# Performance work log

Measured on AMD Instinct MI355X. Metric: run time of the kernel, lower is better.

The kernel has to match this reference:

```python
import jax, jax.numpy as jnp
import numpy as np

B, T, D, H, E, DLAT = 4, 2048, 512, 8, 32, 64
DH = D // H  # head_dim = 64


def rmsnorm(x, gamma, eps=1e-6):
    norm = jnp.sqrt(jnp.mean(jnp.square(x), axis=-1, keepdims=True) + eps)
    return gamma * (x / norm)


def apply_rope(x):
    # x: (B, T, H, Dh); rotate-half style RoPE over last dim
    _, t, _, d = x.shape
    inv_freq = 1.0 / (10000.0 ** (jnp.arange(0, d, 2, dtype=jnp.float32) / d))
    freqs = jnp.outer(jnp.arange(t, dtype=jnp.float32), inv_freq)  # (T, d/2)
    sin = jnp.sin(freqs)[None, :, None, :]
    cos = jnp.cos(freqs)[None, :, None, :]
    x1, x2 = jnp.split(x, 2, axis=-1)
    return jnp.concatenate([x1 * cos - x2 * sin, x1 * sin + x2 * cos], axis=-1)


def setup_inputs() -> dict:
    key = jax.random.key(0)
    ks = jax.random.split(key, 8)
    s = lambda fan_in: 1.0 / np.sqrt(fan_in)
    return {
        "x": jax.random.normal(ks[0], (B, T, D), jnp.float32),
        "gamma1": jnp.ones((D,), jnp.float32),
        "gamma2": jnp.ones((D,), jnp.float32),
        "wq": jax.random.normal(ks[1], (D, D), jnp.float32) * s(D),
        "bq": jnp.zeros((D,), jnp.float32),
        "wkd": jax.random.normal(ks[2], (D, DLAT), jnp.float32) * s(D),
        "bkd": jnp.zeros((DLAT,), jnp.float32),
        "wku": jax.random.normal(ks[3], (DLAT, 2 * D), jnp.float32) * s(DLAT),
        "bku": jnp.zeros((2 * D,), jnp.float32),
        "wo": jax.random.normal(ks[4], (D, D), jnp.float32) * s(D),
        "bo": jnp.zeros((D,), jnp.float32),
        "wg": jax.random.normal(ks[5], (D, E), jnp.float32) * s(D),
        "bg": jnp.zeros((E,), jnp.float32),
        "expert_w": jax.random.normal(ks[6], (E, D, D), jnp.float32) * s(D),
    }


def reference(x, gamma1, gamma2, wq, bq, wkd, bkd, wku, bku, wo, bo, wg, bg, expert_w):
    b, t, d = x.shape
    # --- MLA attention branch ---
    h = rmsnorm(x, gamma1)
    q = (h @ wq + bq).reshape(b, t, H, DH)
    kv = ((h @ wkd + bkd) @ wku + bku).reshape(b, t, H, 2 * DH)
    k, v = jnp.split(kv, 2, axis=-1)
    q = apply_rope(q)
    k = apply_rope(k)
    # NOTE (faithful to source): attention is across HEADS per timestep -> (B,T,H,H)
    att = jnp.einsum("bthd,btgd->bthg", q, k) / jnp.sqrt(jnp.float32(DH))
    att = jax.nn.softmax(att, axis=-1)
    out = jnp.einsum("bthg,btgd->bthd", att, v).reshape(b, t, d)
    x = x + (out @ wo + bo)
    # --- dense soft-MoE branch ---
    h2 = rmsnorm(x, gamma2)
    gate = jax.nn.softmax(h2 @ wg + bg, axis=-1)  # (B, T, E)
    moe = jnp.einsum("btd,edf,bte->btf", h2, expert_w, gate)
    return x + moe
```

## Files before the change

kernel.cpp:

```cpp
#include <hip/hip_runtime.h>
#include <hip/hip_bf16.h>

#define B_ 4
#define T_ 2048
#define D_ 512
#define H_ 8
#define E_ 32
#define DLAT_ 64
#define DH_ 64
#define M_ (B_*T_)

typedef unsigned short u16;
typedef unsigned int u32;
typedef __bf16 bf16x8 __attribute__((ext_vector_type(8)));
typedef float f32x4 __attribute__((ext_vector_type(4)));

__device__ __forceinline__ float bf2f(u16 u) {
    union { u32 i; float f; } c; c.i = ((u32)u) << 16; return c.f;
}
__device__ __forceinline__ u16 f2bf(float f) {
    union { float f; u32 i; } c; c.f = f;
    u32 x = c.i; x += 0x7fffu + ((x >> 16) & 1u);
    return (u16)(x >> 16);
}
__device__ __forceinline__ u32 pack2(float a, float b) {
    return (u32)f2bf(a) | ((u32)f2bf(b) << 16);
}

__global__ __launch_bounds__(256) void transpose_f2b(
    const float* __restrict__ src, u16* __restrict__ dst,
    int R, int C, int dstStride, long srcBatchStride, int dstBatchOff)
{
    __shared__ float tile[32][33];
    const int z = blockIdx.z;
    const float* s = src + (long)z * srcBatchStride;
    const int c0 = blockIdx.x * 32, r0 = blockIdx.y * 32;
    const int tx = threadIdx.x, ty = threadIdx.y;
#pragma unroll
    for (int i = 0; i < 32; i += 8) {
        int r = r0 + ty + i, c = c0 + tx;
        if (r < R && c < C) tile[ty + i][tx] = s[(long)r * C + c];
    }
    __syncthreads();
#pragma unroll
    for (int i = 0; i < 32; i += 8) {
        int c = c0 + ty + i, r = r0 + tx;
        if (r < R && c < C)
            dst[(long)c * dstStride + (long)z * dstBatchOff + r] = f2bf(tile[tx][ty + i]);
    }
}

__global__ __launch_bounds__(256) void rmsnorm_k(
    const float* __restrict__ x, const float* __restrict__ gamma,
    float* __restrict__ of, u16* __restrict__ ob)
{
    const size_t row = blockIdx.x;
    const int t = threadIdx.x;
    const float* xr = x + row * D_;
    float2 v = *(const float2*)(xr + 2 * t);
    float ss = v.x * v.x + v.y * v.y;
#pragma unroll
    for (int off = 1; off < 64; off <<= 1) ss += __shfl_xor(ss, off, 64);
    __shared__ float wsum[4];
    if ((t & 63) == 0) wsum[t >> 6] = ss;
    __syncthreads();
    float tot = wsum[0] + wsum[1] + wsum[2] + wsum[3];
    float inv = rsqrtf(tot * (1.0f / D_) + 1e-6f);
    float o0 = v.x * inv * gamma[2 * t];
    float o1 = v.y * inv * gamma[2 * t + 1];
    if (of) *(float2*)(of + row * D_ + 2 * t) = make_float2(o0, o1);
    if (ob) *(u32*)(ob + row * D_ + 2 * t) = pack2(o0, o1);
}

__global__ __launch_bounds__(512, 4) void gemm8w(
    const u16* __restrict__ A, const u16* __restrict__ Bt,
    const float* __restrict__ bias, const float* __restrict__ resid,
    float* __restrict__ outF, u16* __restrict__ outB, int Ndim, int strideA, int K)
{
    __shared__ __align__(16) u16 lA[128][72];
    __shared__ __align__(16) u16 lB[128][72];
    const int t = threadIdx.x;
    const int lane = t & 63, wid = t >> 6;
    const int wr = wid >> 2, wc = wid & 3;
    const int rowBase = blockIdx.x * 128;
    const int colBase = blockIdx.y * 128;
    const int srow = t >> 3;
    const int scol = (t & 7) * 8;
    const int l15 = lane & 15;
    const int kreg = (lane >> 4) * 8;

    f32x4 acc[4][2] = {};

    for (int kb = 0; kb < K; kb += 64) {
#pragma unroll
        for (int i = 0; i < 2; ++i) {
            int r = srow + 64 * i;
            *(int4*)(&lA[r][scol]) =
                *(const int4*)(A + (size_t)(rowBase + r) * strideA + kb + scol);
            *(int4*)(&lB[r][scol]) =
                *(const int4*)(Bt + (size_t)(colBase + r) * K + kb + scol);
        }
        __syncthreads();
#pragma unroll
        for (int kk = 0; kk < 64; kk += 32) {
            const int ko = kk + kreg;
            bf16x8 af[4], bfr[2];
#pragma unroll
            for (int mi = 0; mi < 4; ++mi)
                af[mi] = *(const bf16x8*)(&lA[wr * 64 + mi * 16 + l15][ko]);
#pragma unroll
            for (int ni = 0; ni < 2; ++ni)
                bfr[ni] = *(const bf16x8*)(&lB[wc * 32 + ni * 16 + l15][ko]);
#pragma unroll
            for (int mi = 0; mi < 4; ++mi)
#pragma unroll
                for (int ni = 0; ni < 2; ++ni)
                    acc[mi][ni] = __builtin_amdgcn_mfma_f32_16x16x32_bf16(
                        af[mi], bfr[ni], acc[mi][ni], 0, 0, 0);
        }
        __syncthreads();
    }
#pragma unroll
    for (int mi = 0; mi < 4; ++mi)
#pragma unroll
        for (int ni = 0; ni < 2; ++ni)
#pragma unroll
            for (int r = 0; r < 4; ++r) {
                int grow = rowBase + wr * 64 + mi * 16 + (lane >> 4) * 4 + r;
                int gcol = colBase + wc * 32 + ni * 16 + l15;
                float v = acc[mi][ni][r];
                if (bias)  v += bias[gcol];
                if (resid) v += resid[(size_t)grow * Ndim + gcol];
                if (outF)  outF[(size_t)grow * Ndim + gcol] = v;
                if (outB)  outB[(size_t)grow * Ndim + gcol] = f2bf(v);
            }
}

#define KPS_ 4096
__global__ __launch_bounds__(512, 4) void moe256(
    const u16* __restrict__ A, const u16* __restrict__ Bt,
    const float* __restrict__ gate, const float* __restrict__ resid,
    float* __restrict__ part)
{
    __shared__ __align__(16) u16 lA[256][72];
    __shared__ __align__(16) u16 lB[128][72];
    const int t = threadIdx.x;
    const int lane = t & 63, wid = t >> 6;
    const int wr = wid >> 1, wc = wid & 1;
    const int rowBase = blockIdx.x * 256;
    const int colBase = blockIdx.y * 128;
    const int z = blockIdx.z;
    const int eBase = z * (KPS_ / 512);
    float* outF = part + (size_t)z * M_ * D_;
    const float* rz = (z == 0) ? resid : nullptr;
    const int srow = t >> 3;
    const int scol = (t & 7) * 8;
    const int l15 = lane & 15;
    const int kreg = (lane >> 4) * 8;

    f32x4 acc[4][4] = {};

    for (int ei = 0; ei < 8; ++ei) {
        const int e = eBase + ei;
        float g[4];
#pragma unroll
        for (int i = 0; i < 4; ++i)
            g[i] = gate[(size_t)(rowBase + srow + 64 * i) * E_ + e];
#pragma unroll 1
        for (int k8 = 0; k8 < 8; ++k8) {
            const int akb = k8 * 64;
            const int kb = e * 512 + akb;
#pragma unroll
            for (int i = 0; i < 4; ++i) {
                int r = srow + 64 * i;
                bf16x8 raw = *(const bf16x8*)(A + (size_t)(rowBase + r) * 512 + akb + scol);
                bf16x8 o;
#pragma unroll
                for (int j = 0; j < 8; ++j)
                    o[j] = (__bf16)((float)raw[j] * g[i]);
                *(bf16x8*)(&lA[r][scol]) = o;
            }
#pragma unroll
            for (int i = 0; i < 2; ++i) {
                int r = srow + 64 * i;
                *(int4*)(&lB[r][scol]) =
                    *(const int4*)(Bt + (size_t)(colBase + r) * (E_ * 512) + kb + scol);
            }
            __syncthreads();
#pragma unroll
            for (int kk = 0; kk < 64; kk += 32) {
                const int ko = kk + kreg;
                bf16x8 af[4], bfr[4];
#pragma unroll
                for (int mi = 0; mi < 4; ++mi)
                    af[mi] = *(const bf16x8*)(&lA[wr * 64 + mi * 16 + l15][ko]);
#pragma unroll
                for (int ni = 0; ni < 4; ++ni)
                    bfr[ni] = *(const bf16x8*)(&lB[wc * 64 + ni * 16 + l15][ko]);
#pragma unroll
                for (int mi = 0; mi < 4; ++mi)
#pragma unroll
                    for (int ni = 0; ni < 4; ++ni)
                        acc[mi][ni] = __builtin_amdgcn_mfma_f32_16x16x32_bf16(
                            af[mi], bfr[ni], acc[mi][ni], 0, 0, 0);
            }
            __syncthreads();
        }
    }
#pragma unroll
    for (int mi = 0; mi < 4; ++mi)
#pragma unroll
        for (int ni = 0; ni < 4; ++ni)
#pragma unroll
            for (int r = 0; r < 4; ++r) {
                int grow = rowBase + wr * 64 + mi * 16 + (lane >> 4) * 4 + r;
                int gcol = colBase + wc * 64 + ni * 16 + l15;
                float v = acc[mi][ni][r];
                if (rz) v += rz[(size_t)grow * D_ + gcol];
                outF[(size_t)grow * D_ + gcol] = v;
            }
}

__global__ __launch_bounds__(256) void gemm_bt(
    const u16* __restrict__ A, const u16* __restrict__ Bt,
    const float* __restrict__ bias, float* __restrict__ outF,
    u16* __restrict__ outB, int Ndim, int K)
{
    __shared__ __align__(16) u16 lA[128][72];
    __shared__ __align__(16) u16 lB[64][72];
    const int t = threadIdx.x;
    const int lane = t & 63, wid = t >> 6;
    const int rowBase = blockIdx.x * 128;
    const int colBase = blockIdx.y * 64;
    const int srow = t >> 3;
    const int skb = (t & 7) * 8;
    const int l15 = lane & 15;
    const int kreg = (lane >> 4) * 8;

    f32x4 accT[2][4] = {};

    for (int kb = 0; kb < K; kb += 64) {
#pragma unroll
        for (int i = 0; i < 4; ++i) {
            int r = srow + 32 * i;
            size_t grow = (size_t)(rowBase + r);
            *(int4*)(&lA[r][skb]) = *(const int4*)(A + grow * (size_t)K + kb + skb);
        }
#pragma unroll
        for (int i = 0; i < 2; ++i) {
            int n = srow + 32 * i;
            int gn = colBase + n;
            int4 v = {0, 0, 0, 0};
            if (gn < Ndim) v = *(const int4*)(Bt + (size_t)gn * K + kb + skb);
            *(int4*)(&lB[n][skb]) = v;
        }
        __syncthreads();
#pragma unroll
        for (int kk = 0; kk < 64; kk += 32) {
            const int ko = kk + kreg;
            bf16x8 af[2], bfr[4];
            af[0] = *(const bf16x8*)(&lA[wid * 32 + l15][ko]);
            af[1] = *(const bf16x8*)(&lA[wid * 32 + 16 + l15][ko]);
#pragma unroll
            for (int ni = 0; ni < 4; ++ni)
                bfr[ni] = *(const bf16x8*)(&lB[ni * 16 + l15][ko]);
#pragma unroll
            for (int mi = 0; mi < 2; ++mi)
#pragma unroll
                for (int ni = 0; ni < 4; ++ni)
                    accT[mi][ni] = __builtin_amdgcn_mfma_f32_16x16x32_bf16(
                        af[mi], bfr[ni], accT[mi][ni], 0, 0, 0);
        }
        __syncthreads();
    }
#pragma unroll
    for (int mi = 0; mi < 2; ++mi)
#pragma unroll
        for (int ni = 0; ni < 4; ++ni)
#pragma unroll
            for (int r = 0; r < 4; ++r) {
                int grow = rowBase + wid * 32 + mi * 16 + (lane >> 4) * 4 + r;
                int gcol = colBase + ni * 16 + l15;
                if (gcol < Ndim) {
                    float v = accT[mi][ni][r];
                    if (bias)  v += bias[gcol];
                    if (outF)  outF[(size_t)grow * Ndim + gcol] = v;
                    if (outB)  outB[(size_t)grow * Ndim + gcol] = f2bf(v);
                }
            }
}

__global__ __launch_bounds__(256) void gatefused_k(
    const u16* __restrict__ A, const u16* __restrict__ Bt,
    const float* __restrict__ bg, float* __restrict__ gate)
{
    __shared__ __align__(16) u16 lA[128][72];
    __shared__ __align__(16) u16 lB[32][72];
    const int t = threadIdx.x;
    const int lane = t & 63, wid = t >> 6;
    const int rowBase = blockIdx.x * 128;
    const int srow = t >> 3;
    const int skb = (t & 7) * 8;
    const int l15 = lane & 15;
    const int kreg = (lane >> 4) * 8;

    f32x4 accT[2][2] = {};

    for (int kb = 0; kb < 512; kb += 64) {
#pragma unroll
        for (int i = 0; i < 4; ++i) {
            int r = srow + 32 * i;
            *(int4*)(&lA[r][skb]) =
                *(const int4*)(A + (size_t)(rowBase + r) * 512 + kb + skb);
        }
        *(int4*)(&lB[srow][skb]) = *(const int4*)(Bt + (size_t)srow * 512 + kb + skb);
        __syncthreads();
#pragma unroll
        for (int kk = 0; kk < 64; kk += 32) {
            const int ko = kk + kreg;
            bf16x8 af[2], bfr[2];
            af[0] = *(const bf16x8*)(&lA[wid * 32 + l15][ko]);
            af[1] = *(const bf16x8*)(&lA[wid * 32 + 16 + l15][ko]);
#pragma unroll
            for (int ni = 0; ni < 2; ++ni)
                bfr[ni] = *(const bf16x8*)(&lB[ni * 16 + l15][ko]);
#pragma unroll
            for (int mi = 0; mi < 2; ++mi)
#pragma unroll
                for (int ni = 0; ni < 2; ++ni)
                    accT[mi][ni] = __builtin_amdgcn_mfma_f32_16x16x32_bf16(
                        af[mi], bfr[ni], accT[mi][ni], 0, 0, 0);
        }
        __syncthreads();
    }
#pragma unroll
    for (int mi = 0; mi < 2; ++mi)
#pragma unroll
        for (int r = 0; r < 4; ++r) {
            float v0 = accT[mi][0][r] + bg[l15];
            float v1 = accT[mi][1][r] + bg[16 + l15];
            float m = fmaxf(v0, v1);
#pragma unroll
            for (int off = 1; off < 16; off <<= 1) m = fmaxf(m, __shfl_xor(m, off, 64));
            float p0 = __expf(v0 - m), p1 = __expf(v1 - m);
            float den = p0 + p1;
#pragma unroll
            for (int off = 1; off < 16; off <<= 1) den += __shfl_xor(den, off, 64);
            float rinv = 1.0f / den;
            int grow = rowBase + wid * 32 + mi * 16 + (lane >> 4) * 4 + r;
            gate[(size_t)grow * E_ + l15] = p0 * rinv;
            gate[(size_t)grow * E_ + 16 + l15] = p1 * rinv;
        }
}

__global__ __launch_bounds__(256) void reduce4_k(
    const float* __restrict__ p, float* __restrict__ o, int n4)
{
    int i = blockIdx.x * 256 + threadIdx.x;
    const int stride = gridDim.x * 256;
    for (; i < n4; i += stride) {
        float4 v0 = ((const float4*)p)[i];
        float4 v1 = ((const float4*)p)[i + n4];
        float4 v2 = ((const float4*)p)[i + 2 * n4];
        float4 v3 = ((const float4*)p)[i + 3 * n4];
        float4 r;
        r.x = v0.x + v1.x + v2.x + v3.x;
        r.y = v0.y + v1.y + v2.y + v3.y;
        r.z = v0.z + v1.z + v2.z + v3.z;
        r.w = v0.w + v1.w + v2.w + v3.w;
        ((float4*)o)[i] = r;
    }
}

__global__ __launch_bounds__(256) void rope_build(float2* __restrict__ tab)
{
    int i = blockIdx.x * 256 + threadIdx.x;
    int tpos = i >> 5, j = i & 31;
    float inv = exp2f(-(float)j * (13.287712379549449f / 32.0f));
    float ang = (float)tpos * inv;
    float sn, cs;
    sincosf(ang, &sn, &cs);
    tab[i] = make_float2(cs, sn);
}

__global__ __launch_bounds__(64) void attn_k(
    const u16* __restrict__ q, const u16* __restrict__ kv,
    const float2* __restrict__ rope, u16* __restrict__ out)
{
    const int tok = blockIdx.x;
    const int tpos = tok & (T_ - 1);
    const int l = threadIdx.x;
    __shared__ float sq[8][65], sk[8][65], sv[8][65];
    __shared__ float satt[8][9];
    const int h = l >> 3;
    const int j0 = (l & 7) * 4;
    const u16* qr = q + (size_t)tok * 512;
    const u16* kr = kv + (size_t)tok * 1024;
#pragma unroll
    for (int jj = 0; jj < 4; ++jj) {
        int j = j0 + jj;
        float2 cssn = rope[tpos * 32 + j];
        float cs = cssn.x, sn = cssn.y;
        float q1 = bf2f(qr[h * 64 + j]), q2 = bf2f(qr[h * 64 + 32 + j]);
        sq[h][j] = q1 * cs - q2 * sn;
        sq[h][j + 32] = q1 * sn + q2 * cs;
        float k1 = bf2f(kr[h * 128 + j]), k2 = bf2f(kr[h * 128 + 32 + j]);
        sk[h][j] = k1 * cs - k2 * sn;
        sk[h][j + 32] = k1 * sn + k2 * cs;
        sv[h][j] = bf2f(kr[h * 128 + 64 + j]);
        sv[h][j + 32] = bf2f(kr[h * 128 + 96 + j]);
    }
    __syncthreads();
    const int g = l & 7;
    float s = 0.f;
#pragma unroll 8
    for (int c = 0; c < 64; ++c) s += sq[h][c] * sk[g][c];
    s *= 0.125f;
    float m = s;
#pragma unroll
    for (int off = 4; off; off >>= 1) m = fmaxf(m, __shfl_xor(m, off, 8));
    float p = __expf(s - m);
    float den = p;
#pragma unroll
    for (int off = 4; off; off >>= 1) den += __shfl_xor(den, off, 8);
    satt[h][g] = p / den;
    __syncthreads();
    const int c8 = (l & 7) * 8;
    float o[8] = {};
#pragma unroll
    for (int gg = 0; gg < 8; ++gg) {
        float a = satt[h][gg];
#pragma unroll
        for (int i = 0; i < 8; ++i) o[i] += a * sv[gg][c8 + i];
    }
    int4 pk;
    pk.x = pack2(o[0], o[1]); pk.y = pack2(o[2], o[3]);
    pk.z = pack2(o[4], o[5]); pk.w = pack2(o[6], o[7]);
    *(int4*)(out + (size_t)tok * 512 + h * 64 + c8) = pk;
}

extern "C" void kernel_launch(void* const* d_in, const int* in_sizes, int n_in,
                              void* d_out, int out_size, void* d_ws, size_t ws_size,
                              hipStream_t stream)
{
    const float* x      = (const float*)d_in[0];
    const float* gamma1 = (const float*)d_in[1];
    const float* gamma2 = (const float*)d_in[2];
    const float* wq     = (const float*)d_in[3];
    const float* bq     = (const float*)d_in[4];
    const float* wkd    = (const float*)d_in[5];
    const float* bkd    = (const float*)d_in[6];
    const float* wku    = (const float*)d_in[7];
    const float* bku    = (const float*)d_in[8];
    const float* wo     = (const float*)d_in[9];
    const float* bo     = (const float*)d_in[10];
    const float* wg     = (const float*)d_in[11];
    const float* bg     = (const float*)d_in[12];
    const float* expw   = (const float*)d_in[13];

    char* w = (char*)d_ws;
    size_t off = 0;
    auto alloc = [&](size_t bytes) -> void* {
        void* p = w + off; off += (bytes + 255) & ~(size_t)255; return p;
    };
    u16*   h_b    = (u16*)alloc((size_t)M_ * D_ * 2);
    u16*   kd_b   = (u16*)alloc((size_t)M_ * DLAT_ * 2);
    u16*   at_b   = (u16*)alloc((size_t)M_ * D_ * 2);
    u16*   h2_b   = (u16*)alloc((size_t)M_ * D_ * 2);
    u16*   q_b    = (u16*)alloc((size_t)M_ * D_ * 2);
    u16*   kv_b   = (u16*)alloc((size_t)M_ * 2 * D_ * 2);
    float* parts  = (float*)alloc((size_t)4 * M_ * D_ * 4);
    float* x1_f   = (float*)alloc((size_t)M_ * D_ * 4);
    float* gate_f = (float*)alloc((size_t)M_ * E_ * 4);
    float2* rope_t = (float2*)alloc((size_t)T_ * 32 * 8);
    u16*   wqT    = (u16*)alloc((size_t)D_ * D_ * 2);
    u16*   wkdT   = (u16*)alloc((size_t)D_ * DLAT_ * 2);
    u16*   wkuT   = (u16*)alloc((size_t)DLAT_ * 2 * D_ * 2);
    u16*   woT    = (u16*)alloc((size_t)D_ * D_ * 2);
    u16*   wgT    = (u16*)alloc((size_t)D_ * E_ * 2);
    u16*   expT   = (u16*)alloc((size_t)E_ * D_ * D_ * 2);
    (void)ws_size; (void)in_sizes; (void)n_in; (void)out_size;

    dim3 tb(32, 8);
    transpose_f2b<<<dim3(16, 16, 1), tb, 0, stream>>>(wq,  wqT,  512, 512, 512, 0L, 0);
    transpose_f2b<<<dim3(2, 16, 1),  tb, 0, stream>>>(wkd, wkdT, 512, 64,  512, 0L, 0);
    transpose_f2b<<<dim3(32, 2, 1),  tb, 0, stream>>>(wku, wkuT, 64, 1024, 64,  0L, 0);
    transpose_f2b<<<dim3(16, 16, 1), tb, 0, stream>>>(wo,  woT,  512, 512, 512, 0L, 0);
    transpose_f2b<<<dim3(1, 16, 1),  tb, 0, stream>>>(wg,  wgT,  512, 32,  512, 0L, 0);
    transpose_f2b<<<dim3(16, 16, 32), tb, 0, stream>>>(expw, expT, 512, 512, 16384,
                                                       (long)512 * 512, 512);
    rope_build<<<(T_ * 32) / 256, 256, 0, stream>>>(rope_t);
    rmsnorm_k<<<M_, 256, 0, stream>>>(x, gamma1, nullptr, h_b);
    gemm8w<<<dim3(64, 4), 512, 0, stream>>>(h_b, wqT, bq, nullptr, nullptr, q_b,
                                            512, 512, 512);
    gemm_bt<<<dim3(64, 1), 256, 0, stream>>>(h_b, wkdT, bkd, nullptr, kd_b, 64, 512);
    gemm8w<<<dim3(64, 8), 512, 0, stream>>>(kd_b, wkuT, bku, nullptr, nullptr, kv_b,
                                            1024, 64, 64);
    attn_k<<<M_, 64, 0, stream>>>(q_b, kv_b, rope_t, at_b);
    gemm8w<<<dim3(64, 4), 512, 0, stream>>>(at_b, woT, bo, x, x1_f, nullptr,
                                            512, 512, 512);
    rmsnorm_k<<<M_, 256, 0, stream>>>(x1_f, gamma2, nullptr, h2_b);
    gatefused_k<<<dim3(64, 1), 256, 0, stream>>>(h2_b, wgT, bg, gate_f);
    moe256<<<dim3(32, 4, 4), 512, 0, stream>>>(h2_b, expT, gate_f, x1_f, parts);
    reduce4_k<<<2048, 256, 0, stream>>>(parts, (float*)d_out, M_ * D_ / 4);
}
```

Baseline: 342.3 us.

## Merge weight prep launches, store MoE partials in bf16, batch attention tokens

Folds the six weight transposes and the RoPE table build into one prep kernel dispatched by block index, which removes several launch overheads. Three of the four MoE split-K partial outputs are now written and read as bf16 instead of fp32, which cuts partial-sum traffic at some cost in precision. The attention kernel processes four tokens per 256-thread block instead of one token per 64-thread block, which improves occupancy and scheduling.

```diff
diff --git a/kernel.cpp b/kernel.cpp
--- a/kernel.cpp
+++ b/kernel.cpp
@@ -27,15 +27,45 @@
     return (u32)f2bf(a) | ((u32)f2bf(b) << 16);
 }
 
-__global__ __launch_bounds__(256) void transpose_f2b(
-    const float* __restrict__ src, u16* __restrict__ dst,
-    int R, int C, int dstStride, long srcBatchStride, int dstBatchOff)
-{
+__global__ __launch_bounds__(256) void prep_k(
+    const float* __restrict__ wq, const float* __restrict__ wkd,
+    const float* __restrict__ wku, const float* __restrict__ wo,
+    const float* __restrict__ wg, const float* __restrict__ expw,
+    u16* __restrict__ wqT, u16* __restrict__ wkdT, u16* __restrict__ wkuT,
+    u16* __restrict__ woT, u16* __restrict__ wgT, u16* __restrict__ expT,
+    float2* __restrict__ rope)
+{
+    int b = blockIdx.x;
+    if (b >= 8816) {
+        int i = (b - 8816) * 256 + threadIdx.x;
+        int tpos = i >> 5, j = i & 31;
+        float inv = exp2f(-(float)j * (13.287712379549449f / 32.0f));
+        float ang = (float)tpos * inv;
+        float sn, cs;
+        sincosf(ang, &sn, &cs);
+        rope[i] = make_float2(cs, sn);
+        return;
+    }
+    const float* src; u16* dst;
+    int R, C, dstStride, dstBatchOff, bx, by, z = 0;
+    long srcBatch = 0;
+    if (b < 256)      { src = wq;  dst = wqT;  R = 512; C = 512;  dstStride = 512;
+                        dstBatchOff = 0; bx = b & 15; by = b >> 4; }
+    else if (b < 288) { b -= 256; src = wkd; dst = wkdT; R = 512; C = 64; dstStride = 512;
+                        dstBatchOff = 0; bx = b & 1;  by = b >> 1; }
+    else if (b < 352) { b -= 288; src = wku; dst = wkuT; R = 64; C = 1024; dstStride = 64;
+                        dstBatchOff = 0; bx = b & 31; by = b >> 5; }
+    else if (b < 608) { b -= 352; src = wo;  dst = woT;  R = 512; C = 512; dstStride = 512;
+                        dstBatchOff = 0; bx = b & 15; by = b >> 4; }
+    else if (b < 624) { b -= 608; src = wg;  dst = wgT;  R = 512; C = 32;  dstStride = 512;
+                        dstBatchOff = 0; bx = 0;      by = b; }
+    else              { b -= 624; src = expw; dst = expT; R = 512; C = 512; dstStride = 16384;
+                        dstBatchOff = 512; bx = b & 15; by = (b >> 4) & 15; z = b >> 8;
+                        srcBatch = (long)512 * 512; }
     __shared__ float tile[32][33];
-    const int z = blockIdx.z;
-    const float* s = src + (long)z * srcBatchStride;
-    const int c0 = blockIdx.x * 32, r0 = blockIdx.y * 32;
-    const int tx = threadIdx.x, ty = threadIdx.y;
+    const float* s = src + (long)z * srcBatch;
+    const int c0 = bx * 32, r0 = by * 32;
+    const int tx = threadIdx.x & 31, ty = threadIdx.x >> 5;
 #pragma unroll
     for (int i = 0; i < 32; i += 8) {
         int r = r0 + ty + i, c = c0 + tx;
@@ -140,7 +170,7 @@
 __global__ __launch_bounds__(512, 4) void moe256(
     const u16* __restrict__ A, const u16* __restrict__ Bt,
     const float* __restrict__ gate, const float* __restrict__ resid,
-    float* __restrict__ part)
+    float* __restrict__ partF, u16* __restrict__ partB)
 {
     __shared__ __align__(16) u16 lA[256][72];
     __shared__ __align__(16) u16 lB[128][72];
@@ -151,8 +181,8 @@
     const int colBase = blockIdx.y * 128;
     const int z = blockIdx.z;
     const int eBase = z * (KPS_ / 512);
-    float* outF = part + (size_t)z * M_ * D_;
-    const float* rz = (z == 0) ? resid : nullptr;
+    float* outF = (z == 0) ? partF : nullptr;
+    u16* outB = (z == 0) ? nullptr : partB + (size_t)(z - 1) * M_ * D_;
     const int srow = t >> 3;
     const int scol = (t & 7) * 8;
     const int l15 = lane & 15;
@@ -216,8 +246,12 @@
                 int grow = rowBase + wr * 64 + mi * 16 + (lane >> 4) * 4 + r;
                 int gcol = colBase + wc * 64 + ni * 16 + l15;
                 float v = acc[mi][ni][r];
-                if (rz) v += rz[(size_t)grow * D_ + gcol];
-                outF[(size_t)grow * D_ + gcol] = v;
+                if (outF) {
+                    v += resid[(size_t)grow * D_ + gcol];
+                    outF[(size_t)grow * D_ + gcol] = v;
+                } else {
+                    outB[(size_t)grow * D_ + gcol] = f2bf(v);
+                }
             }
 }
 
@@ -353,45 +387,34 @@
         }
 }
 
-__global__ __launch_bounds__(256) void reduce4_k(
-    const float* __restrict__ p, float* __restrict__ o, int n4)
+__global__ __launch_bounds__(256) void reduceP_k(
+    const float* __restrict__ pf, const u16* __restrict__ pb,
+    float* __restrict__ o, int n4)
 {
     int i = blockIdx.x * 256 + threadIdx.x;
     const int stride = gridDim.x * 256;
     for (; i < n4; i += stride) {
-        float4 v0 = ((const float4*)p)[i];
-        float4 v1 = ((const float4*)p)[i + n4];
-        float4 v2 = ((const float4*)p)[i + 2 * n4];
-        float4 v3 = ((const float4*)p)[i + 3 * n4];
-        float4 r;
-        r.x = v0.x + v1.x + v2.x + v3.x;
-        r.y = v0.y + v1.y + v2.y + v3.y;
-        r.z = v0.z + v1.z + v2.z + v3.z;
-        r.w = v0.w + v1.w + v2.w + v3.w;
-        ((float4*)o)[i] = r;
-    }
-}
-
-__global__ __launch_bounds__(256) void rope_build(float2* __restrict__ tab)
-{
-    int i = blockIdx.x * 256 + threadIdx.x;
-    int tpos = i >> 5, j = i & 31;
-    float inv = exp2f(-(float)j * (13.287712379549449f / 32.0f));
-    float ang = (float)tpos * inv;
-    float sn, cs;
-    sincosf(ang, &sn, &cs);
-    tab[i] = make_float2(cs, sn);
-}
-
-__global__ __launch_bounds__(64) void attn_k(
+        float4 v = ((const float4*)pf)[i];
+#pragma unroll
+        for (int s = 0; s < 3; ++s) {
+            ushort4 u = ((const ushort4*)pb)[i + s * n4];
+            v.x += bf2f(u.x); v.y += bf2f(u.y);
+            v.z += bf2f(u.z); v.w += bf2f(u.w);
+        }
+        ((float4*)o)[i] = v;
+    }
+}
+
+__global__ __launch_bounds__(256) void attn_k(
     const u16* __restrict__ q, const u16* __restrict__ kv,
     const float2* __restrict__ rope, u16* __restrict__ out)
 {
-    const int tok = blockIdx.x;
+    const int wv = threadIdx.x >> 6;
+    const int tok = blockIdx.x * 4 + wv;
     const int tpos = tok & (T_ - 1);
-    const int l = threadIdx.x;
-    __shared__ float sq[8][65], sk[8][65], sv[8][65];
-    __shared__ float satt[8][9];
+    const int l = threadIdx.x & 63;
+    __shared__ float sq[4][8][65], sk[4][8][65], sv[4][8][65];
+    __shared__ float satt[4][8][9];
     const int h = l >> 3;
     const int j0 = (l & 7) * 4;
     const u16* qr = q + (size_t)tok * 512;
@@ -402,19 +425,19 @@
         float2 cssn = rope[tpos * 32 + j];
         float cs = cssn.x, sn = cssn.y;
         float q1 = bf2f(qr[h * 64 + j]), q2 = bf2f(qr[h * 64 + 32 + j]);
-        sq[h][j] = q1 * cs - q2 * sn;
-        sq[h][j + 32] = q1 * sn + q2 * cs;
+        sq[wv][h][j] = q1 * cs - q2 * sn;
+        sq[wv][h][j + 32] = q1 * sn + q2 * cs;
         float k1 = bf2f(kr[h * 128 + j]), k2 = bf2f(kr[h * 128 + 32 + j]);
-        sk[h][j] = k1 * cs - k2 * sn;
-        sk[h][j + 32] = k1 * sn + k2 * cs;
-        sv[h][j] = bf2f(kr[h * 128 + 64 + j]);
-        sv[h][j + 32] = bf2f(kr[h * 128 + 96 + j]);
+        sk[wv][h][j] = k1 * cs - k2 * sn;
+        sk[wv][h][j + 32] = k1 * sn + k2 * cs;
+        sv[wv][h][j] = bf2f(kr[h * 128 + 64 + j]);
+        sv[wv][h][j + 32] = bf2f(kr[h * 128 + 96 + j]);
     }
     __syncthreads();
     const int g = l & 7;
     float s = 0.f;
 #pragma unroll 8
-    for (int c = 0; c < 64; ++c) s += sq[h][c] * sk[g][c];
+    for (int c = 0; c < 64; ++c) s += sq[wv][h][c] * sk[wv][g][c];
     s *= 0.125f;
     float m = s;
 #pragma unroll
@@ -423,15 +446,15 @@
     float den = p;
 #pragma unroll
     for (int off = 4; off; off >>= 1) den += __shfl_xor(den, off, 8);
-    satt[h][g] = p / den;
+    satt[wv][h][g] = p / den;
     __syncthreads();
     const int c8 = (l & 7) * 8;
     float o[8] = {};
 #pragma unroll
     for (int gg = 0; gg < 8; ++gg) {
-        float a = satt[h][gg];
-#pragma unroll
-        for (int i = 0; i < 8; ++i) o[i] += a * sv[gg][c8 + i];
+        float a = satt[wv][h][gg];
+#pragma unroll
+        for (int i = 0; i < 8; ++i) o[i] += a * sv[wv][gg][c8 + i];
     }
     int4 pk;
     pk.x = pack2(o[0], o[1]); pk.y = pack2(o[2], o[3]);
@@ -469,7 +492,8 @@
     u16*   h2_b   = (u16*)alloc((size_t)M_ * D_ * 2);
     u16*   q_b    = (u16*)alloc((size_t)M_ * D_ * 2);
     u16*   kv_b   = (u16*)alloc((size_t)M_ * 2 * D_ * 2);
-    float* parts  = (float*)alloc((size_t)4 * M_ * D_ * 4);
+    float* partF  = (float*)alloc((size_t)M_ * D_ * 4);
+    u16*   partB  = (u16*)alloc((size_t)3 * M_ * D_ * 2);
     float* x1_f   = (float*)alloc((size_t)M_ * D_ * 4);
     float* gate_f = (float*)alloc((size_t)M_ * E_ * 4);
     float2* rope_t = (float2*)alloc((size_t)T_ * 32 * 8);
@@ -481,26 +505,20 @@
     u16*   expT   = (u16*)alloc((size_t)E_ * D_ * D_ * 2);
     (void)ws_size; (void)in_sizes; (void)n_in; (void)out_size;
 
-    dim3 tb(32, 8);
-    transpose_f2b<<<dim3(16, 16, 1), tb, 0, stream>>>(wq,  wqT,  512, 512, 512, 0L, 0);
-    transpose_f2b<<<dim3(2, 16, 1),  tb, 0, stream>>>(wkd, wkdT, 512, 64,  512, 0L, 0);
-    transpose_f2b<<<dim3(32, 2, 1),  tb, 0, stream>>>(wku, wkuT, 64, 1024, 64,  0L, 0);
-    transpose_f2b<<<dim3(16, 16, 1), tb, 0, stream>>>(wo,  woT,  512, 512, 512, 0L, 0);
-    transpose_f2b<<<dim3(1, 16, 1),  tb, 0, stream>>>(wg,  wgT,  512, 32,  512, 0L, 0);
-    transpose_f2b<<<dim3(16, 16, 32), tb, 0, stream>>>(expw, expT, 512, 512, 16384,
-                                                       (long)512 * 512, 512);
-    rope_build<<<(T_ * 32) / 256, 256, 0, stream>>>(rope_t);
+    prep_k<<<9072, 256, 0, stream>>>(wq, wkd, wku, wo, wg, expw,
+                                     wqT, wkdT, wkuT, woT, wgT, expT, rope_t);
     rmsnorm_k<<<M_, 256, 0, stream>>>(x, gamma1, nullptr, h_b);
     gemm8w<<<dim3(64, 4), 512, 0, stream>>>(h_b, wqT, bq, nullptr, nullptr, q_b,
                                             512, 512, 512);
     gemm_bt<<<dim3(64, 1), 256, 0, stream>>>(h_b, wkdT, bkd, nullptr, kd_b, 64, 512);
     gemm8w<<<dim3(64, 8), 512, 0, stream>>>(kd_b, wkuT, bku, nullptr, nullptr, kv_b,
                                             1024, 64, 64);
-    attn_k<<<M_, 64, 0, stream>>>(q_b, kv_b, rope_t, at_b);
+    attn_k<<<M_ / 4, 256, 0, stream>>>(q_b, kv_b, rope_t, at_b);
     gemm8w<<<dim3(64, 4), 512, 0, stream>>>(at_b, woT, bo, x, x1_f, nullptr,
                                             512, 512, 512);
     rmsnorm_k<<<M_, 256, 0, stream>>>(x1_f, gamma2, nullptr, h2_b);
     gatefused_k<<<dim3(64, 1), 256, 0, stream>>>(h2_b, wgT, bg, gate_f);
-    moe256<<<dim3(32, 4, 4), 512, 0, stream>>>(h2_b, expT, gate_f, x1_f, parts);
-    reduce4_k<<<2048, 256, 0, stream>>>(parts, (float*)d_out, M_ * D_ / 4);
-}
+    moe256<<<dim3(32, 4, 4), 512, 0, stream>>>(h2_b, expT, gate_f, x1_f,
+                                               partF, partB);
+    reduceP_k<<<2048, 256, 0, stream>>>(partF, partB, (float*)d_out, M_ * D_ / 4);
+}
```

After: 323.9 us (median of 2 runs). 5.4% less time.
